# Kernel tuning notes

Measured on AMD Instinct MI355X. Metric: run time of the kernel, lower is better.

Reference implementation:

```python
import jax, jax.numpy as jnp
import numpy as np

IN_C, OUT_C = 128, 256
KH, KW = 3, 3
STRIDE = (1, 1)
PAD = (1, 1)


def setup_inputs() -> dict:
    key = jax.random.key(0)
    kx, kw = jax.random.split(key)
    x = jax.random.normal(kx, (32, IN_C, 56, 56), dtype=jnp.float32)
    k = 1.0 / (IN_C * KH * KW)
    weight = (2.0 * jax.random.uniform(kw, (OUT_C, IN_C, KH, KW), dtype=jnp.float32) - 1.0) * (k ** 0.5)
    return {"x": x, "weight": weight}


def reference(x, weight):
    # Equivalent to the as_strided broadcast-multiply-sum: a plain 2D cross-correlation
    # (no bias), NCHW input, OIHW weight, stride (1,1), padding (1,1).
    return jax.lax.conv_general_dilated(
        x, weight,
        window_strides=STRIDE,
        padding=[(PAD[0], PAD[0]), (PAD[1], PAD[1])],
        dimension_numbers=("NCHW", "OIHW", "NCHW"),
    )
```

## Files before the change

### kernel.cpp

```cpp
#include <hip/hip_runtime.h>

typedef __attribute__((ext_vector_type(8))) short short8;
typedef __attribute__((ext_vector_type(4))) float floatx4;

#define IN_C 128
#define OUT_C 256
#define NB 32
#define HW 56
#define S_PER_N (HW * HW)
#define M_TOTAL (NB * S_PER_N)
#define PH 58
#define PW 66
#define XN_ELEMS (NB * PH * PW * IN_C)
#define WT_ELEMS (9 * OUT_C * IN_C)

__device__ __forceinline__ unsigned short f2bf(float f) {
    unsigned int u = __builtin_bit_cast(unsigned int, f);
    u = (u + 0x7FFFu + ((u >> 16) & 1u)) >> 16;
    return (unsigned short)u;
}

__device__ __forceinline__ void gld_lds16(const unsigned short* g, unsigned short* l) {
    __builtin_amdgcn_global_load_lds(
        (const __attribute__((address_space(1))) unsigned int*)g,
        (__attribute__((address_space(3))) unsigned int*)l, 16, 0, 0);
}

__global__ void xform_x(const float* __restrict__ x, unsigned short* __restrict__ xn) {
    const int ihp = blockIdx.x;
    const int n   = blockIdx.y;
    const int tid = threadIdx.x;
    unsigned int* __restrict__ row32 =
        (unsigned int*)(xn + (size_t)(n * PH + ihp) * PW * IN_C);
    const int WORDS = PW * IN_C / 2;

    if (ihp == 0 || ihp == PH - 1) {
        for (int i = tid; i < WORDS; i += 256) row32[i] = 0u;
        return;
    }
    const int ih = ihp - 1;
    __shared__ unsigned short lds2[HW][IN_C];
    const float* __restrict__ xrow = x + (size_t)n * IN_C * S_PER_N + (size_t)ih * HW;
    for (int i = tid; i < IN_C * 14; i += 256) {
        int ic = i / 14, iw4 = (i % 14) * 4;
        float4 v = *(const float4*)(xrow + (size_t)ic * S_PER_N + iw4);
        lds2[iw4 + 0][ic] = f2bf(v.x);
        lds2[iw4 + 1][ic] = f2bf(v.y);
        lds2[iw4 + 2][ic] = f2bf(v.z);
        lds2[iw4 + 3][ic] = f2bf(v.w);
    }
    __syncthreads();
    for (int wi = tid; wi < WORDS; wi += 256) {
        int pix = wi >> 6;
        int icw = wi & 63;
        unsigned int val = 0u;
        if (pix >= 1 && pix <= HW)
            val = *(const unsigned int*)&lds2[pix - 1][icw * 2];
        row32[wi] = val;
    }
}

__global__ void xform_w(const float* __restrict__ w, unsigned short* __restrict__ wt) {
    const int idx = blockIdx.x * 256 + threadIdx.x;
    const int ic  = idx & 127;
    const int oc  = (idx >> 7) & 255;
    const int khw = idx >> 15;
    wt[idx] = f2bf(w[(oc * IN_C + ic) * 9 + khw]);
}

__global__ void __launch_bounds__(256, 3)
conv_mfma(const unsigned short* __restrict__ xn,
          const unsigned short* __restrict__ wt,
          float* __restrict__ out) {
    const int tid  = threadIdx.x;
    const int lane = tid & 63;
    const int wv   = tid >> 6;
    const int l15  = lane & 15;
    const int quad = lane >> 4;

    const int bx      = blockIdx.x;
    const int tile_oc = bx & 1;
    const int tile_m  = bx >> 1;

    const int s_blk  = tile_m * 128;
    const int oc_blk = tile_oc * 128;
    const int s0  = s_blk + (wv & 1) * 64;
    const int oc0 = oc_blk + (wv >> 1) * 64;

    __shared__ unsigned short A_lds[128 * 64];
    __shared__ unsigned short B_lds[128 * 64];

    const int srow = tid >> 3;
    const int sic  = (tid & 7) * 8;

    const unsigned short* a_g[4];
    const unsigned short* b_g[4];
#pragma unroll
    for (int q = 0; q < 4; ++q) {
        int row = q * 32 + srow;
        a_g[q] = wt + (size_t)(oc_blk + row) * IN_C + sic;
        int sg = s_blk + row;
        int n  = sg / S_PER_N;
        int r  = sg % S_PER_N;
        int oh = r / HW, ow = r % HW;
        b_g[q] = xn + (size_t)((n * PH + oh) * PW + ow) * IN_C + sic;
    }
    unsigned short* a_l = A_lds + tid * 8;
    unsigned short* b_l = B_lds + tid * 8;

    int afo[4], bfo[4];
#pragma unroll
    for (int i = 0; i < 4; ++i)
        afo[i] = ((wv >> 1) * 64 + i * 16 + l15) * 64 + quad * 8;
#pragma unroll
    for (int j = 0; j < 4; ++j)
        bfo[j] = ((wv & 1) * 64 + j * 16 + l15) * 64 + quad * 8;

    floatx4 acc[4][4];
#pragma unroll
    for (int i = 0; i < 4; ++i)
#pragma unroll
        for (int j = 0; j < 4; ++j) acc[i][j] = (floatx4){0.f, 0.f, 0.f, 0.f};

#pragma unroll
    for (int khw = 0; khw < 9; ++khw) {
        const int xo = ((khw / 3) * PW + (khw % 3)) * IN_C;
        const int wo = khw * OUT_C * IN_C;
#pragma unroll
        for (int h = 0; h < 2; ++h) {
            const int ic0 = h * 64;
            __syncthreads();
#pragma unroll
            for (int q = 0; q < 4; ++q) {
                gld_lds16(a_g[q] + wo + ic0, a_l + q * 2048);
                gld_lds16(b_g[q] + xo + ic0, b_l + q * 2048);
            }
            __syncthreads();

#pragma unroll
            for (int kk = 0; kk < 2; ++kk) {
                const int ko = kk * 32;
                short8 a[4], b[4];
#pragma unroll
                for (int i = 0; i < 4; ++i) a[i] = *(const short8*)(A_lds + afo[i] + ko);
#pragma unroll
                for (int j = 0; j < 4; ++j) b[j] = *(const short8*)(B_lds + bfo[j] + ko);
#pragma unroll
                for (int i = 0; i < 4; ++i)
#pragma unroll
                    for (int j = 0; j < 4; ++j)
                        acc[i][j] = __builtin_amdgcn_mfma_f32_16x16x32_bf16(
                            a[i], b[j], acc[i][j], 0, 0, 0);
            }
        }
    }

#pragma unroll
    for (int j = 0; j < 4; ++j) {
        int s_glob = s0 + j * 16 + l15;
        int n = s_glob / S_PER_N;
        int s = s_glob % S_PER_N;
        float* obase = out + (size_t)n * OUT_C * S_PER_N + s;
#pragma unroll
        for (int i = 0; i < 4; ++i) {
            int oc = oc0 + i * 16 + quad * 4;
#pragma unroll
            for (int r = 0; r < 4; ++r)
                obase[(size_t)(oc + r) * S_PER_N] = acc[i][j][r];
        }
    }
}

extern "C" void kernel_launch(void* const* d_in, const int* in_sizes, int n_in,
                              void* d_out, int out_size, void* d_ws, size_t ws_size,
                              hipStream_t stream) {
    const float* x = (const float*)d_in[0];
    const float* w = (const float*)d_in[1];
    float* out = (float*)d_out;

    unsigned short* xn = (unsigned short*)d_ws;
    unsigned short* wt = xn + XN_ELEMS;

    dim3 gx(PH, NB);
    xform_x<<<gx, 256, 0, stream>>>(x, xn);
    xform_w<<<WT_ELEMS / 256, 256, 0, stream>>>(w, wt);
    conv_mfma<<<(M_TOTAL / 128) * 2, 256, 0, stream>>>(xn, wt, out);
}
```

Measured before the change: 217.4 us.

## Double-buffer LDS in 32-wide K chunks with XOR-swizzled layout

The conv GEMM main loop is restructured from 18 single-buffered 64-wide K steps, each with two barriers, into 36 steps of 32-wide K chunks over two LDS buffers. The global-to-LDS load for step t+1 is issued right after the barrier and overlaps the MFMAs of step t, leaving one barrier per step. The 16-byte chunks within each 32-element LDS row are XOR-swizzled by row index to cut LDS bank conflicts on the fragment reads. In exchange there are twice as many loop iterations and barriers relative to the math, and overlap depends on the barrier's vmcnt wait leaving the next load in flight.

```diff
diff --git a/kernel.cpp b/kernel.cpp
--- a/kernel.cpp
+++ b/kernel.cpp
@@ -87,17 +87,18 @@
     const int s0  = s_blk + (wv & 1) * 64;
     const int oc0 = oc_blk + (wv >> 1) * 64;
 
-    __shared__ unsigned short A_lds[128 * 64];
-    __shared__ unsigned short B_lds[128 * 64];
+    __shared__ unsigned short A_lds[2 * 128 * 32];
+    __shared__ unsigned short B_lds[2 * 128 * 32];
 
-    const int srow = tid >> 3;
-    const int sic  = (tid & 7) * 8;
+    const int srow = tid >> 2;
+    const int ci   = tid & 3;
+    const int sic  = (ci ^ (srow & 3)) * 8;
 
-    const unsigned short* a_g[4];
-    const unsigned short* b_g[4];
+    const unsigned short* a_g[2];
+    const unsigned short* b_g[2];
 #pragma unroll
-    for (int q = 0; q < 4; ++q) {
-        int row = q * 32 + srow;
+    for (int q = 0; q < 2; ++q) {
+        int row = q * 64 + srow;
         a_g[q] = wt + (size_t)(oc_blk + row) * IN_C + sic;
         int sg = s_blk + row;
         int n  = sg / S_PER_N;
@@ -108,13 +109,14 @@
     unsigned short* a_l = A_lds + tid * 8;
     unsigned short* b_l = B_lds + tid * 8;
 
-    int afo[4], bfo[4];
+    int arow[4], brow[4];
 #pragma unroll
     for (int i = 0; i < 4; ++i)
-        afo[i] = ((wv >> 1) * 64 + i * 16 + l15) * 64 + quad * 8;
+        arow[i] = ((wv >> 1) * 64 + i * 16 + l15) * 32;
 #pragma unroll
     for (int j = 0; j < 4; ++j)
-        bfo[j] = ((wv & 1) * 64 + j * 16 + l15) * 64 + quad * 8;
+        brow[j] = ((wv & 1) * 64 + j * 16 + l15) * 32;
+    const int koff = (quad ^ (l15 & 3)) * 8;
 
     floatx4 acc[4][4];
 #pragma unroll
@@ -122,37 +124,37 @@
 #pragma unroll
         for (int j = 0; j < 4; ++j) acc[i][j] = (floatx4){0.f, 0.f, 0.f, 0.f};
 
+    auto issue = [&](int t, int buf) {
+        int khw = t >> 2;
+        int sub = (t & 3) * 32;
+        int xo = ((khw / 3) * PW + (khw % 3)) * IN_C + sub;
+        int wo = khw * OUT_C * IN_C + sub;
+        int lb = buf * 4096;
 #pragma unroll
-    for (int khw = 0; khw < 9; ++khw) {
-        const int xo = ((khw / 3) * PW + (khw % 3)) * IN_C;
-        const int wo = khw * OUT_C * IN_C;
+        for (int q = 0; q < 2; ++q) {
+            gld_lds16(a_g[q] + wo, a_l + lb + q * 2048);
+            gld_lds16(b_g[q] + xo, b_l + lb + q * 2048);
+        }
+    };
+
+    issue(0, 0);
 #pragma unroll
-        for (int h = 0; h < 2; ++h) {
-            const int ic0 = h * 64;
-            __syncthreads();
+    for (int t = 0; t < 36; ++t) {
+        __syncthreads();
+        if (t < 35) issue(t + 1, (t + 1) & 1);
+        const unsigned short* Ab = A_lds + (t & 1) * 4096;
+        const unsigned short* Bb = B_lds + (t & 1) * 4096;
+        short8 a[4], b[4];
 #pragma unroll
-            for (int q = 0; q < 4; ++q) {
-                gld_lds16(a_g[q] + wo + ic0, a_l + q * 2048);
-                gld_lds16(b_g[q] + xo + ic0, b_l + q * 2048);
-            }
-            __syncthreads();
-
+        for (int i = 0; i < 4; ++i) a[i] = *(const short8*)(Ab + arow[i] + koff);
 #pragma unroll
-            for (int kk = 0; kk < 2; ++kk) {
-                const int ko = kk * 32;
-                short8 a[4], b[4];
+        for (int j = 0; j < 4; ++j) b[j] = *(const short8*)(Bb + brow[j] + koff);
 #pragma unroll
-                for (int i = 0; i < 4; ++i) a[i] = *(const short8*)(A_lds + afo[i] + ko);
+        for (int i = 0; i < 4; ++i)
 #pragma unroll
-                for (int j = 0; j < 4; ++j) b[j] = *(const short8*)(B_lds + bfo[j] + ko);
-#pragma unroll
-                for (int i = 0; i < 4; ++i)
-#pragma unroll
-                    for (int j = 0; j < 4; ++j)
-                        acc[i][j] = __builtin_amdgcn_mfma_f32_16x16x32_bf16(
-                            a[i], b[j], acc[i][j], 0, 0, 0);
-            }
-        }
+            for (int j = 0; j < 4; ++j)
+                acc[i][j] = __builtin_amdgcn_mfma_f32_16x16x32_bf16(
+                    a[i], b[j], acc[i][j], 0, 0, 0);
     }
 
 #pragma unroll
```

Measured after the change: 218.4 us. No clear change (+0.5%).
